# Kernel optimization log

Hardware: AMD Instinct MI355X
Metric: run time of the kernel (lower is better)

Reference implementation:

```python
import jax, jax.numpy as jnp
import numpy as np

B, S, D, H = 4, 1024, 512, 8
EPS = 1e-5


def _cx(x):
    # [..., 2] float -> complex
    return jax.lax.complex(x[..., 0], x[..., 1])


def setup_inputs() -> dict:
    key = jax.random.key(0)
    ks = jax.random.split(key, 9)
    f = lambda k, sh: jax.random.normal(k, sh, dtype=jnp.float32)
    inp = {
        "q": f(ks[0], (B, S, D, 2)),
        "k": f(ks[1], (B, S, D, 2)),
        "v": f(ks[2], (B, S, D, 2)),
        "Wq": f(ks[3], (D, D, 2)) * 0.02,
        "bq": f(ks[4], (D, 2)) * 0.02,
        "Wk": f(ks[5], (D, D, 2)) * 0.02,
        "bk": f(ks[6], (D, 2)) * 0.02,
        "Wv": f(ks[7], (D, D, 2)) * 0.02,
        "bv": f(ks[8], (D, 2)) * 0.02,
        "gamma_r": jnp.ones((D,), jnp.float32),
        "beta_r": jnp.zeros((D,), jnp.float32),
        "gamma_i": jnp.ones((D,), jnp.float32),
        "beta_i": jnp.zeros((D,), jnp.float32),
        "n_heads": H,
    }
    return inp


def _layernorm(x, g, b):
    # torch LayerNorm: biased variance, eps inside sqrt
    mu = jnp.mean(x, axis=-1, keepdims=True)
    var = jnp.mean((x - mu) ** 2, axis=-1, keepdims=True)
    return (x - mu) / jnp.sqrt(var + EPS) * g + b


def reference(q, k, v, Wq, bq, Wk, bk, Wv, bv, gamma_r, beta_r, gamma_i, beta_i, n_heads):
    qc, kc, vc = _cx(q), _cx(k), _cx(v)
    # complex linear: x @ W^T + b
    Q = jnp.einsum("bsd,ed->bse", qc, _cx(Wq)) + _cx(bq)
    K = jnp.einsum("bsd,ed->bse", kc, _cx(Wk)) + _cx(bk)
    V = jnp.einsum("bsd,ed->bse", vc, _cx(Wv)) + _cx(bv)
    b, s, d = qc.shape
    dh = d // n_heads
    Qh = Q.reshape(b, s, n_heads, dh)
    Kh = K.reshape(b, s, n_heads, dh)
    Vh = V.reshape(b, s, n_heads, dh)
    # complex scores [b,h,q,k], scaled by sqrt(dh)
    scores = jnp.einsum("bqhd,bkhd->bhqk", Qh, Kh) / jnp.sqrt(jnp.float32(dh))
    # original: softmax over view_as_real dim=-2 == key axis, real & imag independently
    attn = jax.lax.complex(jax.nn.softmax(scores.real, axis=-1),
                           jax.nn.softmax(scores.imag, axis=-1))
    # (dropout is identity in eval mode)
    out = jnp.einsum("bhqk,bkhd->bqhd", attn, Vh).reshape(b, s, d)
    out = out + qc  # residual
    out_r = _layernorm(out.real, gamma_r, beta_r)
    out_i = _layernorm(out.imag, gamma_i, beta_i)
    return jnp.stack([out_r, out_i], axis=-1)  # [B,S,D,2]
```

## Files before the change

### kernel.cpp

```cpp
#include <hip/hip_runtime.h>
#include <math.h>

#define BB  4
#define SS  1024
#define DD  512
#define HH  8
#define DHD 64
#define PL  2097152
#define WPL 262144

constexpr float LN_EPS = 1e-5f;

using half4 = __attribute__((ext_vector_type(4))) _Float16;
using half8 = __attribute__((ext_vector_type(8))) _Float16;
using f32x4 = __attribute__((ext_vector_type(4))) float;

__device__ __forceinline__ half8 negh(half8 a) {
    union { half8 h; unsigned int u[4]; } t;
    t.h = a;
    #pragma unroll
    for (int i = 0; i < 4; ++i) t.u[i] ^= 0x80008000u;
    return t.h;
}
__device__ __forceinline__ half8 ldh64(const unsigned short* p, int row, int col) {
    return *(const half8*)(p + row * 64 + (col ^ ((row & 7) << 3)));
}
__device__ __forceinline__ unsigned int cvtpk(float a, float b) {
    union { decltype(__builtin_amdgcn_cvt_pkrtz(0.f, 0.f)) v; unsigned int u; } t;
    t.v = __builtin_amdgcn_cvt_pkrtz(a, b);
    return t.u;
}
#define MFMA16(acc, a, b) acc = __builtin_amdgcn_mfma_f32_16x16x32_f16(a, b, acc, 0, 0, 0)

__global__ __launch_bounds__(256)
void cvt_kernel(const float2* __restrict__ s0, const float2* __restrict__ s1,
                const float2* __restrict__ s2, unsigned short* __restrict__ dst,
                int planeElems) {
    const int z = blockIdx.y;
    const float2* src = z == 0 ? s0 : (z == 1 ? s1 : s2);
    unsigned short* base = dst + (size_t)z * 2 * planeElems;
    const int idx = (blockIdx.x * 256 + threadIdx.x) * 2;
    float4 t = *(const float4*)(src + idx);
    const int m = idx >> 9;
    const int d = idx & 511;
    const int ob = (((m >> 7) << 3) + (d >> 6)) * 8192 + ((m & 127) << 6) + (d & 63);
    union { _Float16 h[2]; unsigned int u; } r, i;
    r.h[0] = (_Float16)t.x; r.h[1] = (_Float16)t.z;
    i.h[0] = (_Float16)t.y; i.h[1] = (_Float16)t.w;
    *(unsigned int*)(base + ob) = r.u;
    *(unsigned int*)(base + planeElems + ob) = i.u;
}

__global__ __launch_bounds__(256, 2)
void proj_kernel(const unsigned short* __restrict__ XP,
                 const unsigned short* __restrict__ WP,
                 const float2* __restrict__ bq, const float2* __restrict__ bk,
                 const float2* __restrict__ bv,
                 unsigned short* __restrict__ QG, unsigned short* __restrict__ KG,
                 unsigned short* __restrict__ VG) {
    const unsigned short* XR = XP + (size_t)blockIdx.z * 2 * PL;
    const unsigned short* XI = XR + PL;
    const unsigned short* WRp = WP + (size_t)blockIdx.z * 2 * WPL;
    const unsigned short* WIp = WRp + WPL;
    const float2* bias; unsigned short* outP;
    if (blockIdx.z == 0)      { bias = bq; outP = QG; }
    else if (blockIdx.z == 1) { bias = bk; outP = KG; }
    else                      { bias = bv; outP = VG; }
    const bool isV = (blockIdx.z == 2);

    __shared__ __align__(16) unsigned short Xs[2][128 * 64];
    __shared__ __align__(16) unsigned short Ws[2][128 * 64];

    const int tid  = threadIdx.x;
    const int w    = tid >> 6;
    const int lane = tid & 63;
    const int quad = lane >> 4;
    const int l15  = lane & 15;
    const int wm   = w >> 1;
    const int we   = w & 1;
    const int m0   = blockIdx.x * 128;
    const int e0   = blockIdx.y * 128;

    const int srow = lane >> 3;
    const int sg   = lane & 7;
    const unsigned short* gplane;
    unsigned short* lb;
    int row0;
    if (w == 0)      { gplane = XR;  row0 = m0; lb = &Xs[0][0]; }
    else if (w == 1) { gplane = XI;  row0 = m0; lb = &Xs[1][0]; }
    else if (w == 2) { gplane = WRp; row0 = e0; lb = &Ws[0][0]; }
    else             { gplane = WIp; row0 = e0; lb = &Ws[1][0]; }
    const unsigned short* gs = gplane + (size_t)row0 * DD + srow * 64 + ((sg ^ srow) << 3);

    f32x4 Sr[4][4], Si[4][4];
    #pragma unroll
    for (int a = 0; a < 4; ++a)
        #pragma unroll
        for (int c = 0; c < 4; ++c) { Sr[a][c] = (f32x4)0.f; Si[a][c] = (f32x4)0.f; }

    for (int s = 0; s < 8; ++s) {
        if (s) __syncthreads();
        const unsigned short* _g = gs + (size_t)s * 8192;
        #pragma unroll
        for (int j = 0; j < 16; ++j)
            __builtin_amdgcn_global_load_lds(
                (const __attribute__((address_space(1))) void*)(_g + j * 512),
                (__attribute__((address_space(3))) void*)(lb + j * 512),
                16, 0, 0);
        __syncthreads();

        #pragma unroll
        for (int kc = 0; kc < 2; ++kc) {
            const int dl = kc * 32 + quad * 8;
            half8 xr[4], xi[4];
            #pragma unroll
            for (int mf = 0; mf < 4; ++mf) {
                const int mr = wm * 64 + mf * 16 + l15;
                xr[mf] = ldh64(Xs[0], mr, dl);
                xi[mf] = ldh64(Xs[1], mr, dl);
            }
            #pragma unroll
            for (int ef = 0; ef < 4; ++ef) {
                const int er = we * 64 + ef * 16 + l15;
                half8 wr  = ldh64(Ws[0], er, dl);
                half8 wi  = ldh64(Ws[1], er, dl);
                half8 wmi = negh(wi);
                #pragma unroll
                for (int mf = 0; mf < 4; ++mf) {
                    MFMA16(Sr[mf][ef], xr[mf], wr);
                    MFMA16(Sr[mf][ef], xi[mf], wmi);
                    MFMA16(Si[mf][ef], xr[mf], wi);
                    MFMA16(Si[mf][ef], xi[mf], wr);
                }
            }
        }
    }

    #pragma unroll
    for (int ef = 0; ef < 4; ++ef) {
        const int eg  = e0 + we * 64 + ef * 16 + l15;
        const int hh  = eg >> 6;
        const int col = eg & 63;
        float2 bb = bias[eg];
        #pragma unroll
        for (int mf = 0; mf < 4; ++mf) {
            #pragma unroll
            for (int reg = 0; reg < 4; ++reg) {
                int m = m0 + wm * 64 + mf * 16 + quad * 4 + reg;
                int bidx = m >> 10;
                int sidx = m & 1023;
                int bh = bidx * HH + hh;
                union { _Float16 h; unsigned short u; } cr, ci;
                cr.h = (_Float16)(Sr[mf][ef][reg] + bb.x);
                ci.h = (_Float16)(Si[mf][ef][reg] + bb.y);
                size_t o = isV ? ((size_t)bh * DHD + col) * SS + sidx
                               : ((size_t)bh * SS + sidx) * DHD + col;
                outP[0 * PL + o] = cr.u;
                outP[1 * PL + o] = ci.u;
            }
        }
    }
}

#define AWID 72
__global__ __launch_bounds__(256, 2)
void attn_kernel(const unsigned short* __restrict__ QG, const unsigned short* __restrict__ KG,
                 const unsigned short* __restrict__ VG,
                 unsigned short* __restrict__ ObR, unsigned short* __restrict__ ObI) {
    __shared__ __align__(16) unsigned short Ks[2][64 * 64];
    __shared__ __align__(16) unsigned short Vt[2][64 * 64];
    __shared__ __align__(16) unsigned short Ps[2][64 * AWID];
    __shared__ float lbuf[2][2][64];

    const int n   = blockIdx.x;
    const int bh  = (n & 7) * 4 + (n >> 7);
    const int q0  = ((n >> 3) & 15) * 64;
    const int b   = bh >> 3;
    const int h   = bh & 7;

    const int tid  = threadIdx.x;
    const int w    = tid >> 6;
    const int lane = tid & 63;
    const int quad = lane >> 4;
    const int l15  = lane & 15;
    const int sw   = w & 1;
    const int tw   = w >> 1;

    const int srow = lane >> 3;
    const int sg   = lane & 7;
    const unsigned short* bp;
    int jstr, ktmul;
    unsigned short* ld;
    if (w < 2) {
        bp = KG + (size_t)w * PL + (size_t)bh * SS * DHD + srow * DHD + ((sg ^ srow) << 3);
        jstr = 8 * DHD; ktmul = DHD; ld = &Ks[w][0];
    } else {
        bp = VG + (size_t)(w - 2) * PL + (size_t)bh * DHD * SS + srow * SS + ((sg ^ srow) << 3);
        jstr = 8 * SS; ktmul = 1; ld = &Vt[w - 2][0];
    }

    half8 qfr[2][2], qfi[2][2], qfmi[2][2];
    #pragma unroll
    for (int qt = 0; qt < 2; ++qt)
        #pragma unroll
        for (int kc = 0; kc < 2; ++kc) {
            size_t qa = ((size_t)bh * SS + q0 + sw * 32 + qt * 16 + l15) * DHD + kc * 32 + quad * 8;
            qfr[qt][kc]  = *(const half8*)(QG + qa);
            qfi[qt][kc]  = *(const half8*)(QG + PL + qa);
            qfmi[qt][kc] = negh(qfi[qt][kc]);
        }

    f32x4 acc[2][2][4];
    #pragma unroll
    for (int qt = 0; qt < 2; ++qt)
        #pragma unroll
        for (int dt = 0; dt < 2; ++dt)
            #pragma unroll
            for (int p = 0; p < 4; ++p) acc[qt][dt][p] = (f32x4)0.f;
    float lacc[2][2] = {{0.f, 0.f}, {0.f, 0.f}};

    constexpr float EC = 0.18033688011112042f;

    for (int kt = 0; kt < SS; kt += 64) {
        __syncthreads();
        const unsigned short* g = bp + (size_t)kt * ktmul;
        #pragma unroll
        for (int j = 0; j < 8; ++j)
            __builtin_amdgcn_global_load_lds(
                (const __attribute__((address_space(1))) void*)(g + j * jstr),
                (__attribute__((address_space(3))) void*)(ld + j * 512),
                16, 0, 0);
        __syncthreads();

        f32x4 Sr[2][2], Si[2][2];
        #pragma unroll
        for (int a = 0; a < 2; ++a)
            #pragma unroll
            for (int c = 0; c < 2; ++c) { Sr[a][c] = (f32x4)0.f; Si[a][c] = (f32x4)0.f; }
        __builtin_amdgcn_s_setprio(1);
        #pragma unroll
        for (int kc = 0; kc < 2; ++kc) {
            const int dl = kc * 32 + quad * 8;
            #pragma unroll
            for (int kt2 = 0; kt2 < 2; ++kt2) {
                const int krow = tw * 32 + kt2 * 16 + l15;
                half8 akr = ldh64(Ks[0], krow, dl);
                half8 aki = ldh64(Ks[1], krow, dl);
                #pragma unroll
                for (int qt = 0; qt < 2; ++qt) {
                    MFMA16(Sr[kt2][qt], akr, qfr[qt][kc]);
                    MFMA16(Sr[kt2][qt], aki, qfmi[qt][kc]);
                    MFMA16(Si[kt2][qt], aki, qfr[qt][kc]);
                    MFMA16(Si[kt2][qt], akr, qfi[qt][kc]);
                }
            }
        }
        __builtin_amdgcn_s_setprio(0);

        #pragma unroll
        for (int kt2 = 0; kt2 < 2; ++kt2)
            #pragma unroll
            for (int qt = 0; qt < 2; ++qt) {
                float er0 = exp2f(Sr[kt2][qt][0] * EC), er1 = exp2f(Sr[kt2][qt][1] * EC);
                float er2 = exp2f(Sr[kt2][qt][2] * EC), er3 = exp2f(Sr[kt2][qt][3] * EC);
                float ei0 = exp2f(Si[kt2][qt][0] * EC), ei1 = exp2f(Si[kt2][qt][1] * EC);
                float ei2 = exp2f(Si[kt2][qt][2] * EC), ei3 = exp2f(Si[kt2][qt][3] * EC);
                lacc[qt][0] += (er0 + er1) + (er2 + er3);
                lacc[qt][1] += (ei0 + ei1) + (ei2 + ei3);
                const int qrow = sw * 32 + qt * 16 + l15;
                const int kcol = tw * 32 + kt2 * 16 + quad * 4;
                uint2 pr, pi;
                pr.x = cvtpk(er0, er1); pr.y = cvtpk(er2, er3);
                pi.x = cvtpk(ei0, ei1); pi.y = cvtpk(ei2, ei3);
                *(uint2*)&Ps[0][qrow * AWID + kcol] = pr;
                *(uint2*)&Ps[1][qrow * AWID + kcol] = pi;
            }
        __syncthreads();

        #pragma unroll
        for (int kc = 0; kc < 2; ++kc) {
            half8 ap[2][2];
            #pragma unroll
            for (int qt = 0; qt < 2; ++qt) {
                const int qrow = sw * 32 + qt * 16 + l15;
                ap[qt][0] = *(const half8*)&Ps[0][qrow * AWID + kc * 32 + quad * 8];
                ap[qt][1] = *(const half8*)&Ps[1][qrow * AWID + kc * 32 + quad * 8];
            }
            __builtin_amdgcn_s_setprio(1);
            #pragma unroll
            for (int dt = 0; dt < 2; ++dt) {
                const int drow = tw * 32 + dt * 16 + l15;
                half8 bvr = ldh64(Vt[0], drow, kc * 32 + quad * 8);
                half8 bvi = ldh64(Vt[1], drow, kc * 32 + quad * 8);
                #pragma unroll
                for (int qt = 0; qt < 2; ++qt) {
                    MFMA16(acc[qt][dt][0], ap[qt][0], bvr);
                    MFMA16(acc[qt][dt][1], ap[qt][0], bvi);
                    MFMA16(acc[qt][dt][2], ap[qt][1], bvr);
                    MFMA16(acc[qt][dt][3], ap[qt][1], bvi);
                }
            }
            __builtin_amdgcn_s_setprio(0);
        }
    }

    __syncthreads();
    #pragma unroll
    for (int qt = 0; qt < 2; ++qt)
        #pragma unroll
        for (int p = 0; p < 2; ++p) {
            float v = lacc[qt][p];
            v += __shfl_xor(v, 16);
            v += __shfl_xor(v, 32);
            if (lane < 16) lbuf[p][tw][sw * 32 + qt * 16 + lane] = v;
        }
    __syncthreads();

    #pragma unroll
    for (int qt = 0; qt < 2; ++qt)
        #pragma unroll
        for (int reg = 0; reg < 4; ++reg) {
            const int qloc = sw * 32 + qt * 16 + quad * 4 + reg;
            const float ir = 1.f / (lbuf[0][0][qloc] + lbuf[0][1][qloc]);
            const float ii = 1.f / (lbuf[1][0][qloc] + lbuf[1][1][qloc]);
            #pragma unroll
            for (int dt = 0; dt < 2; ++dt) {
                const int d = tw * 32 + dt * 16 + l15;
                union { _Float16 h; unsigned short u; } cr, ci;
                cr.h = (_Float16)(acc[qt][dt][0][reg] * ir - acc[qt][dt][3][reg] * ii);
                ci.h = (_Float16)(acc[qt][dt][1][reg] * ir + acc[qt][dt][2][reg] * ii);
                size_t o = ((size_t)b * SS + q0 + qloc) * DD + h * DHD + d;
                ObR[o] = cr.u;
                ObI[o] = ci.u;
            }
        }
}

__global__ __launch_bounds__(256)
void ln_kernel(const unsigned short* __restrict__ OrP, const unsigned short* __restrict__ OiP,
               const float2* __restrict__ Qin,
               const float* __restrict__ gr, const float* __restrict__ br,
               const float* __restrict__ gi, const float* __restrict__ bi,
               float2* __restrict__ out) {
    const int row = blockIdx.x;
    const int tid = threadIdx.x;
    const size_t base = (size_t)row * DD;
    const int e0 = 2 * tid, e1 = 2 * tid + 1;

    union { unsigned int u; _Float16 h[2]; } tr, ti;
    tr.u = *(const unsigned int*)(OrP + base + e0);
    ti.u = *(const unsigned int*)(OiP + base + e0);
    float2 r0 = Qin[base + e0];
    float2 r1 = Qin[base + e1];
    float xr0 = (float)tr.h[0] + r0.x;
    float xr1 = (float)tr.h[1] + r1.x;
    float xi0 = (float)ti.h[0] + r0.y;
    float xi1 = (float)ti.h[1] + r1.y;

    float sr = xr0 + xr1;
    float si = xi0 + xi1;
    float qr = xr0 * xr0 + xr1 * xr1;
    float qi = xi0 * xi0 + xi1 * xi1;
    #pragma unroll
    for (int off = 32; off > 0; off >>= 1) {
        sr += __shfl_down(sr, off);
        si += __shfl_down(si, off);
        qr += __shfl_down(qr, off);
        qi += __shfl_down(qi, off);
    }
    __shared__ float red[4][4];
    __shared__ float stat[4];
    int lane = tid & 63, wid = tid >> 6;
    if (lane == 0) { red[wid][0] = sr; red[wid][1] = si; red[wid][2] = qr; red[wid][3] = qi; }
    __syncthreads();
    if (tid == 0) {
        sr = red[0][0] + red[1][0] + red[2][0] + red[3][0];
        si = red[0][1] + red[1][1] + red[2][1] + red[3][1];
        qr = red[0][2] + red[1][2] + red[2][2] + red[3][2];
        qi = red[0][3] + red[1][3] + red[2][3] + red[3][3];
        float mur = sr * (1.f / DD), mui = si * (1.f / DD);
        float vr = qr * (1.f / DD) - mur * mur;
        float vi = qi * (1.f / DD) - mui * mui;
        stat[0] = mur; stat[1] = mui;
        stat[2] = rsqrtf(vr + LN_EPS); stat[3] = rsqrtf(vi + LN_EPS);
    }
    __syncthreads();
    float mur = stat[0], mui = stat[1], rsr = stat[2], rsi = stat[3];
    out[base + e0] = make_float2((xr0 - mur) * rsr * gr[e0] + br[e0],
                                 (xi0 - mui) * rsi * gi[e0] + bi[e0]);
    out[base + e1] = make_float2((xr1 - mur) * rsr * gr[e1] + br[e1],
                                 (xi1 - mui) * rsi * gi[e1] + bi[e1]);
}

extern "C" void kernel_launch(void* const* d_in, const int* in_sizes, int n_in,
                              void* d_out, int out_size, void* d_ws, size_t ws_size,
                              hipStream_t stream) {
    const float2* q  = (const float2*)d_in[0];
    const float2* k  = (const float2*)d_in[1];
    const float2* v  = (const float2*)d_in[2];
    const float2* Wq = (const float2*)d_in[3];
    const float2* bq = (const float2*)d_in[4];
    const float2* Wk = (const float2*)d_in[5];
    const float2* bk = (const float2*)d_in[6];
    const float2* Wv = (const float2*)d_in[7];
    const float2* bv = (const float2*)d_in[8];
    const float*  gr = (const float*)d_in[9];
    const float*  br = (const float*)d_in[10];
    const float*  gi = (const float*)d_in[11];
    const float*  bi = (const float*)d_in[12];

    unsigned short* XP  = (unsigned short*)d_ws;
    unsigned short* WP  = XP + (size_t)6 * PL;
    unsigned short* QG  = WP + (size_t)6 * WPL;
    unsigned short* KG  = QG + (size_t)2 * PL;
    unsigned short* VG  = KG + (size_t)2 * PL;
    unsigned short* ObR = VG + (size_t)2 * PL;
    unsigned short* ObI = ObR + (size_t)PL;

    cvt_kernel<<<dim3(4096, 3), 256, 0, stream>>>(q, k, v, XP, PL);
    cvt_kernel<<<dim3(512, 3), 256, 0, stream>>>(Wq, Wk, Wv, WP, WPL);
    proj_kernel<<<dim3(32, 4, 3), 256, 0, stream>>>(XP, WP, bq, bk, bv, QG, KG, VG);
    attn_kernel<<<dim3(512), 256, 0, stream>>>(QG, KG, VG, ObR, ObI);
    ln_kernel<<<dim3(BB * SS), 256, 0, stream>>>(ObR, ObI, q, gr, br, gi, bi, (float2*)d_out);
}
```

Measured before the change: 213.5 us.

## Double-buffer K tiles and overlap K/V loads with QK compute in attention

The attention loop now keeps two K stages in LDS. The next K tile is prefetched while the current one is consumed, and the V tile load is issued at the top of each iteration so it overlaps the QK MFMAs and exp stage. This removes one barrier per iteration and replaces a fully serialized load-then-compute step. It also swaps exp2f for the raw hardware exp2 builtin and drops the s_setprio hints. LDS use grows by the extra K buffer, and correctness relies on the barrier waiting for the async global-to-LDS V loads before the PV stage.

```diff
diff --git a/kernel.cpp b/kernel.cpp
--- a/kernel.cpp
+++ b/kernel.cpp
@@ -30,6 +30,7 @@
     t.v = __builtin_amdgcn_cvt_pkrtz(a, b);
     return t.u;
 }
+__device__ __forceinline__ float ex2(float x) { return __builtin_amdgcn_exp2f(x); }
 #define MFMA16(acc, a, b) acc = __builtin_amdgcn_mfma_f32_16x16x32_f16(a, b, acc, 0, 0, 0)
 
 __global__ __launch_bounds__(256)
@@ -167,7 +168,7 @@
 void attn_kernel(const unsigned short* __restrict__ QG, const unsigned short* __restrict__ KG,
                  const unsigned short* __restrict__ VG,
                  unsigned short* __restrict__ ObR, unsigned short* __restrict__ ObI) {
-    __shared__ __align__(16) unsigned short Ks[2][64 * 64];
+    __shared__ __align__(16) unsigned short Ks[2][2][64 * 64];
     __shared__ __align__(16) unsigned short Vt[2][64 * 64];
     __shared__ __align__(16) unsigned short Ps[2][64 * AWID];
     __shared__ float lbuf[2][2][64];
@@ -188,15 +189,25 @@
 
     const int srow = lane >> 3;
     const int sg   = lane & 7;
-    const unsigned short* bp;
-    int jstr, ktmul;
-    unsigned short* ld;
-    if (w < 2) {
-        bp = KG + (size_t)w * PL + (size_t)bh * SS * DHD + srow * DHD + ((sg ^ srow) << 3);
-        jstr = 8 * DHD; ktmul = DHD; ld = &Ks[w][0];
+    const bool isK = (w < 2);
+    const unsigned short* bpK = nullptr;
+    const unsigned short* bpV = nullptr;
+    unsigned short* ldV = nullptr;
+    if (isK) {
+        bpK = KG + (size_t)w * PL + (size_t)bh * SS * DHD + srow * DHD + ((sg ^ srow) << 3);
     } else {
-        bp = VG + (size_t)(w - 2) * PL + (size_t)bh * DHD * SS + srow * SS + ((sg ^ srow) << 3);
-        jstr = 8 * SS; ktmul = 1; ld = &Vt[w - 2][0];
+        bpV = VG + (size_t)(w - 2) * PL + (size_t)bh * DHD * SS + srow * SS + ((sg ^ srow) << 3);
+        ldV = &Vt[w - 2][0];
+    }
+
+#define GLD(SRC, DST) __builtin_amdgcn_global_load_lds( \
+        (const __attribute__((address_space(1))) void*)(SRC), \
+        (__attribute__((address_space(3))) void*)(DST), 16, 0, 0)
+
+    if (isK) {
+        unsigned short* ld = &Ks[0][w][0];
+        #pragma unroll
+        for (int j = 0; j < 8; ++j) GLD(bpK + j * 8 * DHD, ld + j * 512);
     }
 
     half8 qfr[2][2], qfi[2][2], qfmi[2][2];
@@ -221,31 +232,41 @@
 
     constexpr float EC = 0.18033688011112042f;
 
-    for (int kt = 0; kt < SS; kt += 64) {
-        __syncthreads();
-        const unsigned short* g = bp + (size_t)kt * ktmul;
-        #pragma unroll
-        for (int j = 0; j < 8; ++j)
-            __builtin_amdgcn_global_load_lds(
-                (const __attribute__((address_space(1))) void*)(g + j * jstr),
-                (__attribute__((address_space(3))) void*)(ld + j * 512),
-                16, 0, 0);
-        __syncthreads();
+    __syncthreads();
+
+    const unsigned short* Kr_c = &Ks[0][0][0];
+    const unsigned short* Ki_c = &Ks[0][1][0];
+    const unsigned short* Kr_n = &Ks[1][0][0];
+    const unsigned short* Ki_n = &Ks[1][1][0];
+    unsigned short* kst_nxt = isK ? &Ks[1][w][0] : nullptr;
+    unsigned short* kst_alt = isK ? &Ks[0][w][0] : nullptr;
+
+    for (int t = 0; t < 16; ++t) {
+        if (isK) {
+            if (t < 15) {
+                const unsigned short* g = bpK + (size_t)(t + 1) * 64 * DHD;
+                #pragma unroll
+                for (int j = 0; j < 8; ++j) GLD(g + j * 8 * DHD, kst_nxt + j * 512);
+            }
+        } else {
+            const unsigned short* g = bpV + (size_t)t * 64;
+            #pragma unroll
+            for (int j = 0; j < 8; ++j) GLD(g + j * 8 * SS, ldV + j * 512);
+        }
 
         f32x4 Sr[2][2], Si[2][2];
         #pragma unroll
         for (int a = 0; a < 2; ++a)
             #pragma unroll
             for (int c = 0; c < 2; ++c) { Sr[a][c] = (f32x4)0.f; Si[a][c] = (f32x4)0.f; }
-        __builtin_amdgcn_s_setprio(1);
         #pragma unroll
         for (int kc = 0; kc < 2; ++kc) {
             const int dl = kc * 32 + quad * 8;
             #pragma unroll
             for (int kt2 = 0; kt2 < 2; ++kt2) {
                 const int krow = tw * 32 + kt2 * 16 + l15;
-                half8 akr = ldh64(Ks[0], krow, dl);
-                half8 aki = ldh64(Ks[1], krow, dl);
+                half8 akr = ldh64(Kr_c, krow, dl);
+                half8 aki = ldh64(Ki_c, krow, dl);
                 #pragma unroll
                 for (int qt = 0; qt < 2; ++qt) {
                     MFMA16(Sr[kt2][qt], akr, qfr[qt][kc]);
@@ -255,16 +276,15 @@
                 }
             }
         }
-        __builtin_amdgcn_s_setprio(0);
 
         #pragma unroll
         for (int kt2 = 0; kt2 < 2; ++kt2)
             #pragma unroll
             for (int qt = 0; qt < 2; ++qt) {
-                float er0 = exp2f(Sr[kt2][qt][0] * EC), er1 = exp2f(Sr[kt2][qt][1] * EC);
-                float er2 = exp2f(Sr[kt2][qt][2] * EC), er3 = exp2f(Sr[kt2][qt][3] * EC);
-                float ei0 = exp2f(Si[kt2][qt][0] * EC), ei1 = exp2f(Si[kt2][qt][1] * EC);
-                float ei2 = exp2f(Si[kt2][qt][2] * EC), ei3 = exp2f(Si[kt2][qt][3] * EC);
+                float er0 = ex2(Sr[kt2][qt][0] * EC), er1 = ex2(Sr[kt2][qt][1] * EC);
+                float er2 = ex2(Sr[kt2][qt][2] * EC), er3 = ex2(Sr[kt2][qt][3] * EC);
+                float ei0 = ex2(Si[kt2][qt][0] * EC), ei1 = ex2(Si[kt2][qt][1] * EC);
+                float ei2 = ex2(Si[kt2][qt][2] * EC), ei3 = ex2(Si[kt2][qt][3] * EC);
                 lacc[qt][0] += (er0 + er1) + (er2 + er3);
                 lacc[qt][1] += (ei0 + ei1) + (ei2 + ei3);
                 const int qrow = sw * 32 + qt * 16 + l15;
@@ -286,7 +306,6 @@
                 ap[qt][0] = *(const half8*)&Ps[0][qrow * AWID + kc * 32 + quad * 8];
                 ap[qt][1] = *(const half8*)&Ps[1][qrow * AWID + kc * 32 + quad * 8];
             }
-            __builtin_amdgcn_s_setprio(1);
             #pragma unroll
             for (int dt = 0; dt < 2; ++dt) {
                 const int drow = tw * 32 + dt * 16 + l15;
@@ -300,11 +319,16 @@
                     MFMA16(acc[qt][dt][3], ap[qt][1], bvi);
                 }
             }
-            __builtin_amdgcn_s_setprio(0);
-        }
-    }
-
-    __syncthreads();
+        }
+        __syncthreads();
+
+        const unsigned short* tr;
+        tr = Kr_c; Kr_c = Kr_n; Kr_n = tr;
+        tr = Ki_c; Ki_c = Ki_n; Ki_n = tr;
+        unsigned short* ts = kst_nxt; kst_nxt = kst_alt; kst_alt = ts;
+    }
+#undef GLD
+
     #pragma unroll
     for (int qt = 0; qt < 2; ++qt)
         #pragma unroll
```

After: 205.2 us. 3.9% less time.
